# Kernel optimization log

Measured on AMD Instinct MI355X. Metric: run time of the kernel, lower is better.

The kernel has to match this reference:

```python
import jax, jax.numpy as jnp
import numpy as np

# Circuit dimensions (levelized DAG stand-in for the SDD-derived network)
B = 1024          # batch
NUM_VARS = 2048   # propositional variables
LEAVES = 2 * NUM_VARS  # positive + negative literal nodes (smooth circuit)
LEVELS = 12       # internal levels (topological depth)
WIDTH = 4096      # internal nodes per level
FANIN = 4         # children per internal node
TOTAL = LEAVES + LEVELS * WIDTH  # total nodes in execution order


def setup_inputs() -> dict:
    key = jax.random.key(0)
    x = jax.random.uniform(key, (B, NUM_VARS), dtype=jnp.float32)
    rng = np.random.default_rng(0)
    # child_idx[l, i, k]: index (into the global node-output buffer) of the
    # k-th child of node i at level l. DAG constraint: children must be
    # earlier nodes, i.e. index < LEAVES + l * WIDTH.
    child_idx = np.zeros((LEVELS, WIDTH, FANIN), dtype=np.int32)
    for l in range(LEVELS):
        cap = LEAVES + l * WIDTH
        child_idx[l] = rng.integers(0, cap, size=(WIDTH, FANIN), dtype=np.int32)
    # op_type: 0 -> AND node (product of children), 1 -> OR node (sum of children)
    op_type = rng.integers(0, 2, size=(LEVELS, WIDTH)).astype(np.int32)
    return {"x": x,
            "child_idx": jnp.asarray(child_idx),
            "op_type": jnp.asarray(op_type)}


def reference(x, child_idx, op_type):
    """Bottom-up evaluation of the levelized arithmetic circuit.

    x:         [B, NUM_VARS] literal probabilities
    child_idx: [LEVELS, WIDTH, FANIN] int32 child indices (constants)
    op_type:   [LEVELS, WIDTH] int32, 0=AND (prod), 1=OR (sum)
    Returns:   [B] root node output (last node in execution order).
    """
    b = x.shape[0]
    # Leaf (literal/prob node) outputs: [x, 1-x] -> [B, LEAVES]
    leaf = jnp.concatenate([x, 1.0 - x], axis=1)
    buf = jnp.zeros((b, TOTAL), dtype=x.dtype)
    buf = buf.at[:, :LEAVES].set(leaf)
    n_levels = child_idx.shape[0]
    for l in range(n_levels):  # structural loop over circuit depth (small, fixed)
        ch = buf[:, child_idx[l]]                 # gather children: [B, WIDTH, FANIN]
        out = jnp.where(op_type[l] == 0,
                        jnp.prod(ch, axis=-1),    # AND nodes
                        jnp.sum(ch, axis=-1))     # OR nodes
        start = LEAVES + l * WIDTH
        buf = buf.at[:, start:start + WIDTH].set(out)
    return buf[:, -1]  # root output
```

## Files before the change

kernel.cpp:

```cpp
#include <hip/hip_runtime.h>

#define BATCH    1024
#define NUM_VARS 2048
#define LEAVES   (2 * NUM_VARS)
#define LEVELS   12
#define WIDTH    4096
#define TOTAL    (LEAVES + LEVELS * WIDTH)
#define NWORDS   (TOTAL / 32)
#define NNWORDS  (NWORDS - 128)

#define CAP      2048
#define BSLICE   4
#define NEVB     (BATCH / BSLICE)
#define ETHR     1024

#define ROWS     (NUM_VARS + CAP)
#define LDSTRIDE 4100

#define OFF_BUF   0
#define SZ_BUF    (4 * LDSTRIDE * 4)
#define OFF_ENC   (OFF_BUF + SZ_BUF)
#define SZ_ENC    (CAP * 16)
#define OFF_FLG   (OFF_ENC + SZ_ENC)
#define SZ_FLG    (NWORDS * 4)
#define OFF_NID   (OFF_FLG + SZ_FLG)
#define SZ_NID    ((CAP + 8) * 4)
#define OFF_WSC   (OFF_NID + SZ_NID)
#define SZ_WSC    (NNWORDS * 4)
#define OFF_MISC  (OFF_WSC + SZ_WSC)
#define SMEM_BYTES (OFF_MISC + 128)

#define WARM_N   1536


__global__ __launch_bounds__(ETHR) void fused_kernel(const float* __restrict__ x,
                                                     const int4* __restrict__ child4,
                                                     const int*  __restrict__ op_type,
                                                     float* __restrict__ out)
{
    extern __shared__ char smem[];
    float*        buf      = (float*)(smem + OFF_BUF);
    int4*         enc_s    = (int4*)(smem + OFF_ENC);
    unsigned int* flg      = (unsigned int*)(smem + OFF_FLG);
    int*          nid      = (int*)(smem + OFF_NID);
    int*          wscan    = (int*)(smem + OFF_WSC);
    int*          lvl_cnt  = (int*)(smem + OFF_MISC);
    int*          lvl_base = lvl_cnt + LEVELS;
    int*          total_s  = lvl_base + LEVELS;

    const int tid  = threadIdx.x;
    const int lane = tid & 63;
    const int wv   = tid >> 6;

    const int pc_ = tid >> 8;
    const int pq  = tid & 255;
    const float4* xr4 =
        (const float4*)(x + (size_t)(blockIdx.x * BSLICE + pc_) * NUM_VARS);
    const float4 lf0 = xr4[pq];
    const float4 lf1 = xr4[pq + 256];
    {
        const int seg = (blockIdx.x >> 3) & 31;
        const int4 w0 = child4[seg * WARM_N + tid];
        int acc = w0.x ^ w0.y ^ w0.z ^ w0.w;
        if (tid < WARM_N - 1024) {
            const int4 w1 = child4[seg * WARM_N + 1024 + tid];
            acc ^= w1.x ^ w1.y ^ w1.z ^ w1.w;
        }
        asm volatile("" :: "v"(acc));
    }

    for (int i = tid; i < NWORDS; i += ETHR)
        flg[i] = (i == NWORDS - 1) ? 0x80000000u : 0u;

    {
        float* br = buf + pc_ * LDSTRIDE;
        ((float4*)br)[pq]       = lf0;
        ((float4*)br)[pq + 256] = lf1;
    }
    __syncthreads();

    for (int l = LEVELS - 1; l >= 0; --l) {
        const int wbase = 128 * (l + 1);
        const unsigned int fw = flg[wbase + (tid >> 3)];
        const int sh = (tid & 7) * 4;
        int4 c0, c1, c2, c3;
        {
            const int b = l * WIDTH + (tid << 2);
            c0 = child4[((fw >> (sh + 0)) & 1u) ? b + 0 : 0];
            c1 = child4[((fw >> (sh + 1)) & 1u) ? b + 1 : 0];
            c2 = child4[((fw >> (sh + 2)) & 1u) ? b + 2 : 0];
            c3 = child4[((fw >> (sh + 3)) & 1u) ? b + 3 : 0];
        }
        if ((fw >> (sh + 0)) & 1u) {
            atomicOr(&flg[c0.x >> 5], 1u << (c0.x & 31));
            atomicOr(&flg[c0.y >> 5], 1u << (c0.y & 31));
            atomicOr(&flg[c0.z >> 5], 1u << (c0.z & 31));
            atomicOr(&flg[c0.w >> 5], 1u << (c0.w & 31));
        }
        if ((fw >> (sh + 1)) & 1u) {
            atomicOr(&flg[c1.x >> 5], 1u << (c1.x & 31));
            atomicOr(&flg[c1.y >> 5], 1u << (c1.y & 31));
            atomicOr(&flg[c1.z >> 5], 1u << (c1.z & 31));
            atomicOr(&flg[c1.w >> 5], 1u << (c1.w & 31));
        }
        if ((fw >> (sh + 2)) & 1u) {
            atomicOr(&flg[c2.x >> 5], 1u << (c2.x & 31));
            atomicOr(&flg[c2.y >> 5], 1u << (c2.y & 31));
            atomicOr(&flg[c2.z >> 5], 1u << (c2.z & 31));
            atomicOr(&flg[c2.w >> 5], 1u << (c2.w & 31));
        }
        if ((fw >> (sh + 3)) & 1u) {
            atomicOr(&flg[c3.x >> 5], 1u << (c3.x & 31));
            atomicOr(&flg[c3.y >> 5], 1u << (c3.y & 31));
            atomicOr(&flg[c3.z >> 5], 1u << (c3.z & 31));
            atomicOr(&flg[c3.w >> 5], 1u << (c3.w & 31));
        }
        __syncthreads();
    }

    if (wv < LEVELS) {
        const unsigned int w0 = flg[128 * (wv + 1) + 2 * lane];
        const unsigned int w1 = flg[128 * (wv + 1) + 2 * lane + 1];
        const int pc = __popc(w0) + __popc(w1);
        int scan = pc;
        for (int d = 1; d < 64; d <<= 1) {
            const int up = __shfl_up(scan, d, 64);
            if (lane >= d) scan += up;
        }
        if (lane == 63) lvl_cnt[wv] = scan;
    }
    __syncthreads();
    if (tid == 0) {
        int s = 0;
        for (int l = 0; l < LEVELS; ++l) { lvl_base[l] = s; s += lvl_cnt[l]; }
        *total_s = (s < CAP) ? s : CAP;
    }
    __syncthreads();

    if (wv < LEVELS) {
        const unsigned int w0 = flg[128 * (wv + 1) + 2 * lane];
        const unsigned int w1 = flg[128 * (wv + 1) + 2 * lane + 1];
        const int pc = __popc(w0) + __popc(w1);
        int scan = pc;
        for (int d = 1; d < 64; d <<= 1) {
            const int up = __shfl_up(scan, d, 64);
            if (lane >= d) scan += up;
        }
        int base = lvl_base[wv] + scan - pc;
        wscan[128 * wv + 2 * lane]     = base;
        wscan[128 * wv + 2 * lane + 1] = base + __popc(w0);
        const int nd0 = LEAVES + wv * WIDTH + 64 * lane;
        unsigned int w = w0;
        while (w) { const int b = __ffs(w) - 1; w &= w - 1;
                    if (base < CAP) nid[base] = nd0 + b;      base++; }
        w = w1;
        while (w) { const int b = __ffs(w) - 1; w &= w - 1;
                    if (base < CAP) nid[base] = nd0 + 32 + b; base++; }
    }
    __syncthreads();

    const int S = *total_s;
    for (int slot = tid; slot < S; slot += ETHR) {
        const int nd = nid[slot];
        const int4 c = child4[nd - LEAVES];
        const int  o = op_type[nd - LEAVES];
        int4 e;
        {
            const int cc = c.x;
            const int w  = cc >> 5;
            const int r  = (cc >= LEAVES)
                ? NUM_VARS + wscan[w - 128] + __popc(flg[w] & ((1u << (cc & 31)) - 1))
                : (cc < NUM_VARS ? cc : (cc - NUM_VARS) | 0x4000);
            e.x = r;
        }
        {
            const int cc = c.y;
            const int w  = cc >> 5;
            e.y = (cc >= LEAVES)
                ? NUM_VARS + wscan[w - 128] + __popc(flg[w] & ((1u << (cc & 31)) - 1))
                : (cc < NUM_VARS ? cc : (cc - NUM_VARS) | 0x4000);
        }
        {
            const int cc = c.z;
            const int w  = cc >> 5;
            e.z = (cc >= LEAVES)
                ? NUM_VARS + wscan[w - 128] + __popc(flg[w] & ((1u << (cc & 31)) - 1))
                : (cc < NUM_VARS ? cc : (cc - NUM_VARS) | 0x4000);
        }
        {
            const int cc = c.w;
            const int w  = cc >> 5;
            e.w = (cc >= LEAVES)
                ? NUM_VARS + wscan[w - 128] + __popc(flg[w] & ((1u << (cc & 31)) - 1))
                : (cc < NUM_VARS ? cc : (cc - NUM_VARS) | 0x4000);
        }
        e.x |= o << 20;
        enc_s[slot] = e;
    }
    __syncthreads();

    const int col = tid & 3;
    const int nl  = tid >> 2;
    float* bc = buf + col * LDSTRIDE;

    for (int l = 0; l < LEVELS; ++l) {
        const int n  = lvl_cnt[l];
        const int sb = lvl_base[l];
        for (int i = nl; i < n; i += ETHR / BSLICE) {
            const int4 e = enc_s[sb + i];
            float v0 = bc[e.x & 0x3FFF];
            float v1 = bc[e.y & 0x3FFF];
            float v2 = bc[e.z & 0x3FFF];
            float v3 = bc[e.w & 0x3FFF];
            v0 = (e.x & 0x4000) ? 1.0f - v0 : v0;
            v1 = (e.y & 0x4000) ? 1.0f - v1 : v1;
            v2 = (e.z & 0x4000) ? 1.0f - v2 : v2;
            v3 = (e.w & 0x4000) ? 1.0f - v3 : v3;
            const float p = ((v0 * v1) * v2) * v3;
            const float s = ((v0 + v1) + v2) + v3;
            const float r = (e.x & (1 << 20)) ? s : p;
            bc[NUM_VARS + sb + i] = r;
            if (l == LEVELS - 1 && i == n - 1)
                out[blockIdx.x * BSLICE + col] = r;
        }
        __syncthreads();
    }
}

extern "C" void kernel_launch(void* const* d_in, const int* in_sizes, int n_in,
                              void* d_out, int out_size, void* d_ws, size_t ws_size,
                              hipStream_t stream)
{
    const float* x       = (const float*)d_in[0];
    const int4*  child4  = (const int4*)d_in[1];
    const int*   op_type = (const int*)d_in[2];
    float*       out     = (float*)d_out;
    (void)d_ws; (void)ws_size;

    static bool lds_opted = false;
    if (!lds_opted) {
        hipFuncSetAttribute((const void*)fused_kernel,
                            hipFuncAttributeMaxDynamicSharedMemorySize, SMEM_BYTES);
        lds_opted = true;
    }

    fused_kernel<<<NEVB, ETHR, SMEM_BYTES, stream>>>(x, child4, op_type, out);
}
```

Measured before the change: 75.35 us.

## Evaluate each batch column on a single wavefront without block barriers

The circuit-evaluation phase is remapped so that each of the four batch columns is handled by one 64-lane wavefront, and all other waves exit early. Because a column's LDS buffer is now touched by only one wave, the per-level __syncthreads is replaced by a block-scope fence. The loop is also unrolled by two so each lane evaluates two nodes per iteration for more memory-level parallelism. The cost is far fewer active lanes per column, so levels with many active nodes take more serial iterations, and correctness now relies on in-wave ordering of LDS accesses.

```diff
diff --git a/kernel.cpp b/kernel.cpp
--- a/kernel.cpp
+++ b/kernel.cpp
@@ -168,10 +168,9 @@
         {
             const int cc = c.x;
             const int w  = cc >> 5;
-            const int r  = (cc >= LEAVES)
-                ? NUM_VARS + wscan[w - 128] + __popc(flg[w] & ((1u << (cc & 31)) - 1))
-                : (cc < NUM_VARS ? cc : (cc - NUM_VARS) | 0x4000);
-            e.x = r;
+            e.x = (cc >= LEAVES)
+                ? NUM_VARS + wscan[w - 128] + __popc(flg[w] & ((1u << (cc & 31)) - 1))
+                : (cc < NUM_VARS ? cc : (cc - NUM_VARS) | 0x4000);
         }
         {
             const int cc = c.y;
@@ -199,31 +198,45 @@
     }
     __syncthreads();
 
-    const int col = tid & 3;
-    const int nl  = tid >> 2;
-    float* bc = buf + col * LDSTRIDE;
+    if (wv >= BSLICE) return;
+
+    float* bc = buf + wv * LDSTRIDE;
+    const int ob = blockIdx.x * BSLICE + wv;
 
     for (int l = 0; l < LEVELS; ++l) {
         const int n  = lvl_cnt[l];
         const int sb = lvl_base[l];
-        for (int i = nl; i < n; i += ETHR / BSLICE) {
-            const int4 e = enc_s[sb + i];
-            float v0 = bc[e.x & 0x3FFF];
-            float v1 = bc[e.y & 0x3FFF];
-            float v2 = bc[e.z & 0x3FFF];
-            float v3 = bc[e.w & 0x3FFF];
-            v0 = (e.x & 0x4000) ? 1.0f - v0 : v0;
-            v1 = (e.y & 0x4000) ? 1.0f - v1 : v1;
-            v2 = (e.z & 0x4000) ? 1.0f - v2 : v2;
-            v3 = (e.w & 0x4000) ? 1.0f - v3 : v3;
-            const float p = ((v0 * v1) * v2) * v3;
-            const float s = ((v0 + v1) + v2) + v3;
-            const float r = (e.x & (1 << 20)) ? s : p;
-            bc[NUM_VARS + sb + i] = r;
-            if (l == LEVELS - 1 && i == n - 1)
-                out[blockIdx.x * BSLICE + col] = r;
-        }
-        __syncthreads();
+        for (int i = lane; i < n; i += 128) {
+            const int  i2 = i + 64;
+            const bool u2 = (i2 < n);
+            const int4 e1 = enc_s[sb + i];
+            const int4 e2 = enc_s[sb + (u2 ? i2 : i)];
+            float a0 = bc[e1.x & 0x3FFF], a1 = bc[e1.y & 0x3FFF];
+            float a2 = bc[e1.z & 0x3FFF], a3 = bc[e1.w & 0x3FFF];
+            float b0 = bc[e2.x & 0x3FFF], b1 = bc[e2.y & 0x3FFF];
+            float b2 = bc[e2.z & 0x3FFF], b3 = bc[e2.w & 0x3FFF];
+            a0 = (e1.x & 0x4000) ? 1.0f - a0 : a0;
+            a1 = (e1.y & 0x4000) ? 1.0f - a1 : a1;
+            a2 = (e1.z & 0x4000) ? 1.0f - a2 : a2;
+            a3 = (e1.w & 0x4000) ? 1.0f - a3 : a3;
+            const float p1 = ((a0 * a1) * a2) * a3;
+            const float s1 = ((a0 + a1) + a2) + a3;
+            const float r1 = (e1.x & (1 << 20)) ? s1 : p1;
+            bc[NUM_VARS + sb + i] = r1;
+            if (l == LEVELS - 1 && i == n - 1) out[ob] = r1;
+            if (u2) {
+                b0 = (e2.x & 0x4000) ? 1.0f - b0 : b0;
+                b1 = (e2.y & 0x4000) ? 1.0f - b1 : b1;
+                b2 = (e2.z & 0x4000) ? 1.0f - b2 : b2;
+                b3 = (e2.w & 0x4000) ? 1.0f - b3 : b3;
+                const float p2 = ((b0 * b1) * b2) * b3;
+                const float s2 = ((b0 + b1) + b2) + b3;
+                const float r2 = (e2.x & (1 << 20)) ? s2 : p2;
+                bc[NUM_VARS + sb + i2] = r2;
+                if (l == LEVELS - 1 && i2 == n - 1) out[ob] = r2;
+            }
+        }
+        __threadfence_block();
     }
 }
 
```

Measured after the change: 76.78 us. About the same (+1.9%).
